# Kernel tuning notes

Hardware: AMD Instinct MI355X
Metric: run time of the kernel (lower is better)

## Reference

```python
import jax, jax.numpy as jnp
import numpy as np
import math

D_MODEL = 1024
NUM_HEADS = 16
HEAD_DIM = D_MODEL // NUM_HEADS  # 64
THETA = 10000.0
BATCH = 2
SEQ = 2048


def setup_inputs() -> dict:
    key = jax.random.key(0)
    ks = jax.random.split(key, 5)
    scale = 0.02
    return {
        "in_features": jax.random.normal(ks[0], (BATCH, SEQ, D_MODEL), jnp.float32),
        "q_proj": jax.random.normal(ks[1], (D_MODEL, D_MODEL), jnp.float32) * scale,
        "k_proj": jax.random.normal(ks[2], (D_MODEL, D_MODEL), jnp.float32) * scale,
        "v_proj": jax.random.normal(ks[3], (D_MODEL, D_MODEL), jnp.float32) * scale,
        "o_proj": jax.random.normal(ks[4], (D_MODEL, D_MODEL), jnp.float32) * scale,
        "token_positions": jnp.arange(SEQ, dtype=jnp.int32),
    }


def _rope(x, token_positions):
    # x: [b, h, s, head_dim]; interleaved even/odd rotation
    half = HEAD_DIM // 2
    inv_freq = 1.0 / (THETA ** (2.0 * jnp.arange(half, dtype=x.dtype) / HEAD_DIM))
    angle = token_positions.astype(x.dtype)[:, None] * inv_freq[None, :]  # [s, half]
    cos, sin = jnp.cos(angle), jnp.sin(angle)
    x_e, x_o = x[..., ::2], x[..., 1::2]
    r_e = x_e * cos - x_o * sin
    r_o = x_e * sin + x_o * cos
    # interleave back: [..., s, half, 2] -> [..., s, head_dim]
    return jnp.stack([r_e, r_o], axis=-1).reshape(x.shape)


def reference(in_features, q_proj, k_proj, v_proj, o_proj, token_positions):
    b, s, _ = in_features.shape
    # projections: weight layout is [d_out, d_in]
    Q = jnp.einsum('bsd,kd->bsk', in_features, q_proj)
    K = jnp.einsum('bsd,kd->bsk', in_features, k_proj)
    V = jnp.einsum('bsd,kd->bsk', in_features, v_proj)
    # split heads: [b, h, s, head_dim]
    Q = Q.reshape(b, s, NUM_HEADS, HEAD_DIM).transpose(0, 2, 1, 3)
    K = K.reshape(b, s, NUM_HEADS, HEAD_DIM).transpose(0, 2, 1, 3)
    V = V.reshape(b, s, NUM_HEADS, HEAD_DIM).transpose(0, 2, 1, 3)
    Q = _rope(Q, token_positions)
    K = _rope(K, token_positions)
    scores = jnp.einsum('bhnd,bhmd->bhnm', Q, K) / math.sqrt(HEAD_DIM)
    causal = jnp.tril(jnp.ones((s, s), dtype=bool))  # [s, s]
    scores = jnp.where(causal[None, None], scores, -jnp.inf)
    attn = jax.nn.softmax(scores, axis=-1)
    out = jnp.einsum('bhnm,bhmd->bhnd', attn, V)
    out = out.transpose(0, 2, 1, 3).reshape(b, s, D_MODEL)
    return jnp.einsum('bsv,dv->bsd', out, o_proj)
```

## Files before the change

### kernel.cpp

```cpp
#include <hip/hip_runtime.h>
#include <hip/hip_bf16.h>

#define D_MODEL 1024
#define NHEAD   16
#define HDIM    64
#define SEQQ    2048
#define NBATCH  2
#define MROWS   (NBATCH * SEQQ)

typedef unsigned short u16;
typedef __attribute__((ext_vector_type(8))) short short8;
typedef __attribute__((ext_vector_type(4))) short bf16x4;
typedef __attribute__((ext_vector_type(4))) float floatx4;

__device__ __forceinline__ u16 f2b(float f) {
    union { __hip_bfloat16 h; u16 u; } cv;
    cv.h = __float2bfloat16(f);
    return cv.u;
}
__device__ __forceinline__ float b2f(u16 u) {
    return __uint_as_float(((unsigned int)u) << 16);
}
__device__ __forceinline__ short8 load8(const u16* p) {
    return *reinterpret_cast<const short8*>(p);
}
__device__ __forceinline__ bf16x4 load4v(const u16* p) {
    return *reinterpret_cast<const bf16x4*>(p);
}
__device__ __forceinline__ unsigned pack2(float lo, float hi) {
    return ((unsigned)f2b(hi) << 16) | (unsigned)f2b(lo);
}
__device__ __forceinline__ void async_cp16(const void* g, void* l) {
    __builtin_amdgcn_global_load_lds(
        (const __attribute__((address_space(1))) void*)g,
        (__attribute__((address_space(3))) void*)l, 16, 0, 0);
}

__global__ void cvt_all(const float* __restrict__ X,
                        const float* __restrict__ w0, const float* __restrict__ w1,
                        const float* __restrict__ w2, const float* __restrict__ w3,
                        u16* __restrict__ xo,
                        u16* __restrict__ o0, u16* __restrict__ o1,
                        u16* __restrict__ o2, u16* __restrict__ o3) {
    const int z = blockIdx.y;
    const int n4 = (D_MODEL * D_MODEL) / 4;
    const float* in;
    u16* out;
    if (z < 4) { in = X + (size_t)z * n4 * 4;  out = xo + (size_t)z * n4 * 4; }
    else {
        in  = (z == 4) ? w0 : (z == 5) ? w1 : (z == 6) ? w2 : w3;
        out = (z == 4) ? o0 : (z == 5) ? o1 : (z == 6) ? o2 : o3;
    }
    const int i = blockIdx.x * 256 + threadIdx.x;
    float4 v = reinterpret_cast<const float4*>(in)[i];
    ushort4 o;
    o.x = f2b(v.x); o.y = f2b(v.y); o.z = f2b(v.z); o.w = f2b(v.w);
    reinterpret_cast<ushort4*>(out)[i] = o;
}

__global__ __launch_bounds__(256) void gemm_qkv(
    const u16* __restrict__ A,
    const u16* __restrict__ B0, const u16* __restrict__ B1, const u16* __restrict__ B2,
    u16* __restrict__ C0, u16* __restrict__ C1, u16* __restrict__ C2)
{
    const int K = D_MODEL, N = D_MODEL;
    const u16* Bt = (blockIdx.z == 0) ? B0 : (blockIdx.z == 1 ? B1 : B2);
    u16*       Cp = (blockIdx.z == 0) ? C0 : (blockIdx.z == 1 ? C1 : C2);

    __shared__ __attribute__((aligned(16))) u16 As[128 * 32];
    __shared__ __attribute__((aligned(16))) u16 Bs[128 * 32];

    const int tid  = threadIdx.x;
    const int w    = tid >> 6;
    const int lane = tid & 63;
    const int l15  = lane & 15;
    const int quad = lane >> 4;
    const int wm   = w >> 1, wn = w & 1;
    const int tm   = blockIdx.x * 128, tn = blockIdx.y * 128;

    floatx4 acc[4][4];
#pragma unroll
    for (int i = 0; i < 4; i++)
#pragma unroll
        for (int j = 0; j < 4; j++) {
            floatx4 z = {0.f, 0.f, 0.f, 0.f};
            acc[i][j] = z;
        }

    const int srow = lane >> 2;
    const int scol = (lane & 3) * 8;

    for (int k0 = 0; k0 < K; k0 += 32) {
#pragma unroll
        for (int ch = w; ch < 8; ch += 4) {
            async_cp16(A  + (size_t)(tm + ch * 16 + srow) * K + k0 + scol, &As[ch * 512]);
            async_cp16(Bt + (size_t)(tn + ch * 16 + srow) * K + k0 + scol, &Bs[ch * 512]);
        }
        __syncthreads();

        short8 af[4], bfr[4];
#pragma unroll
        for (int mi = 0; mi < 4; mi++)
            af[mi] = load8(&As[(wm * 64 + mi * 16 + l15) * 32 + quad * 8]);
#pragma unroll
        for (int ni = 0; ni < 4; ni++)
            bfr[ni] = load8(&Bs[(wn * 64 + ni * 16 + l15) * 32 + quad * 8]);
#pragma unroll
        for (int mi = 0; mi < 4; mi++)
#pragma unroll
            for (int ni = 0; ni < 4; ni++)
                acc[mi][ni] = __builtin_amdgcn_mfma_f32_16x16x32_bf16(af[mi], bfr[ni], acc[mi][ni], 0, 0, 0);
        __syncthreads();
    }

#pragma unroll
    for (int mi = 0; mi < 4; mi++)
#pragma unroll
        for (int ni = 0; ni < 4; ni++)
#pragma unroll
            for (int rg = 0; rg < 4; rg++) {
                int row = tm + wm * 64 + mi * 16 + quad * 4 + rg;
                int col = tn + wn * 64 + ni * 16 + l15;
                Cp[(size_t)row * N + col] = f2b(acc[mi][ni][rg]);
            }
}

__global__ void rope_qk(const u16* __restrict__ Qraw, const u16* __restrict__ Kraw,
                        const int* __restrict__ pos, u16* __restrict__ Qt, u16* __restrict__ Kt)
{
    const int gid = blockIdx.x * 256 + threadIdx.x;
    const int j = gid & 31;
    const int s = (gid >> 5) & (SEQQ - 1);
    const int h = (gid >> 16) & (NHEAD - 1);
    const int b = gid >> 20;

    const float p   = (float)pos[s];
    const float inv = expf(-(float)j * (9.210340371976184f / 32.0f));
    float sn, cs;
    sincosf(p * inv, &sn, &cs);

    const size_t ioff = ((size_t)(b * SEQQ + s)) * D_MODEL + h * HDIM + 2 * j;
    const ushort2 qp = *reinterpret_cast<const ushort2*>(&Qraw[ioff]);
    const ushort2 kp = *reinterpret_cast<const ushort2*>(&Kraw[ioff]);
    const float qe = b2f(qp.x), qo = b2f(qp.y);
    const float ke = b2f(kp.x), ko = b2f(kp.y);

    const size_t ooff = (((size_t)(b * NHEAD + h)) * SEQQ + s) * HDIM + 2 * j;
    const float qs = 0.18033688011112042f;
    ushort2 qr;
    qr.x = f2b((qe * cs - qo * sn) * qs);
    qr.y = f2b((qe * sn + qo * cs) * qs);
    ushort2 kr;
    kr.x = f2b(ke * cs - ko * sn);
    kr.y = f2b(ke * sn + ko * cs);
    *reinterpret_cast<ushort2*>(&Qt[ooff]) = qr;
    *reinterpret_cast<ushort2*>(&Kt[ooff]) = kr;
}

__global__ __launch_bounds__(256) void vtrans(const u16* __restrict__ Vraw, u16* __restrict__ Vt)
{
    __shared__ u16 tile[64][65];
    const int s0 = blockIdx.x * 64, h = blockIdx.y, b = blockIdx.z;
    const int t = threadIdx.x;
#pragma unroll
    for (int i = 0; i < 16; i++) {
        int idx = t + i * 256;
        int sl = idx >> 6, dl = idx & 63;
        tile[sl][dl] = Vraw[((size_t)(b * SEQQ + s0 + sl)) * D_MODEL + h * HDIM + dl];
    }
    __syncthreads();
#pragma unroll
    for (int i = 0; i < 16; i++) {
        int idx = t + i * 256;
        int dl = idx >> 6, sl = idx & 63;
        Vt[(((size_t)(b * NHEAD + h)) * HDIM + dl) * SEQQ + s0 + sl] = tile[sl][dl];
    }
}

__global__ __launch_bounds__(256, 4) void attn_kernel(
    const u16* __restrict__ Qt, const u16* __restrict__ Kt, const u16* __restrict__ Vt,
    u16* __restrict__ Out)
{
    const int bid = blockIdx.x;
    const int xcd = bid & 7;
    const int u   = bid >> 3;
    const int col = xcd * 4 + (u & 3);
    const int m   = u >> 2;
    int qsub;
    if      (m < 8)  qsub = 31 - m;
    else if (m < 16) qsub = m - 8;
    else if (m < 24) qsub = 39 - m;
    else             qsub = m - 16;
    const int h = col & (NHEAD - 1), b = col >> 4;

    const int tid = threadIdx.x, w = tid >> 6, lane = tid & 63;
    const int l15 = lane & 15, quad = lane >> 4;
    const size_t bh = (size_t)(b * NHEAD + h);
    const u16* Qh = Qt + bh * SEQQ * HDIM;
    const u16* Kh = Kt + bh * SEQQ * HDIM;
    const u16* Vh = Vt + bh * HDIM * SEQQ;

    __shared__ __attribute__((aligned(16))) u16 Ks[2][64 * 64];
    __shared__ __attribute__((aligned(16))) u16 Vs[2][64 * 64];

    short8 ones;
#pragma unroll
    for (int i = 0; i < 8; i++) ones[i] = (short)0x3F80;

    const int rr  = lane >> 3;
    const int swz = ((lane & 7) ^ rr) * 8;
    auto stage = [&](int buf, int tt) {
        const int k0s = tt * 64;
        async_cp16(Kh + (size_t)(k0s + w * 8 + rr) * HDIM + swz,       &Ks[buf][w * 512]);
        async_cp16(Kh + (size_t)(k0s + (w + 4) * 8 + rr) * HDIM + swz, &Ks[buf][(w + 4) * 512]);
        async_cp16(Vh + (size_t)(w * 8 + rr) * SEQQ + k0s + swz,       &Vs[buf][w * 512]);
        async_cp16(Vh + (size_t)((w + 4) * 8 + rr) * SEQQ + k0s + swz, &Vs[buf][(w + 4) * 512]);
    };

    const int s7  = l15 & 7;
    const int sw1 = ((quad)     ^ s7) * 8;
    const int sw2 = ((quad + 4) ^ s7) * 8;
    const int vo0 = (((quad >> 1)    ) ^ s7) * 8 + (quad & 1) * 4;
    const int vo1 = (((quad >> 1) + 2) ^ s7) * 8 + (quad & 1) * 4;
    const int vo2 = (((quad >> 1) + 4) ^ s7) * 8 + (quad & 1) * 4;
    const int vo3 = (((quad >> 1) + 6) ^ s7) * 8 + (quad & 1) * 4;

    const int q0w   = qsub * 64 + w * 16;
    const int tmaxp = qsub;

    short8 qf[2];
#pragma unroll
    for (int kk = 0; kk < 2; kk++)
        qf[kk] = load8(&Qh[(size_t)(q0w + l15) * HDIM + kk * 32 + quad * 8]);

    floatx4 O[4];
    floatx4 l_acc = {0.f, 0.f, 0.f, 0.f};
#pragma unroll
    for (int c = 0; c < 4; c++) { floatx4 z = {0.f, 0.f, 0.f, 0.f}; O[c] = z; }

    stage(0, 0);

    for (int t = 0; t <= tmaxp; ++t) {
        asm volatile("s_waitcnt vmcnt(0)" ::: "memory");
        __builtin_amdgcn_s_barrier();
        if (t < tmaxp) stage((t + 1) & 1, t + 1);

        const u16* KsB = &Ks[t & 1][0];
        const u16* VsB = &Vs[t & 1][0];
        const int k0 = t * 64;

        floatx4 S[4];
#pragma unroll
        for (int c = 0; c < 4; c++) {
            const int rowb = (c * 16 + l15) * 64;
            floatx4 z = {0.f, 0.f, 0.f, 0.f};
            S[c] = __builtin_amdgcn_mfma_f32_16x16x32_bf16(load8(&KsB[rowb + sw1]), qf[0], z,    0, 0, 0);
            S[c] = __builtin_amdgcn_mfma_f32_16x16x32_bf16(load8(&KsB[rowb + sw2]), qf[1], S[c], 0, 0, 0);
        }

        if (t == tmaxp) {
            const int q = q0w + l15;
#pragma unroll
            for (int c = 0; c < 4; c++)
#pragma unroll
                for (int r = 0; r < 4; r++)
                    if (k0 + c * 16 + quad * 4 + r > q) S[c][r] = -1e30f;
        }

#pragma unroll
        for (int c = 0; c < 4; c++)
#pragma unroll
            for (int r = 0; r < 4; r++)
                S[c][r] = __builtin_amdgcn_exp2f(S[c][r]);

        union { short8 v; unsigned u[4]; } pf0, pf1;
        pf0.u[0] = pack2(S[0][0], S[0][1]);
        pf0.u[1] = pack2(S[0][2], S[0][3]);
        pf0.u[2] = pack2(S[1][0], S[1][1]);
        pf0.u[3] = pack2(S[1][2], S[1][3]);
        pf1.u[0] = pack2(S[2][0], S[2][1]);
        pf1.u[1] = pack2(S[2][2], S[2][3]);
        pf1.u[2] = pack2(S[3][0], S[3][1]);
        pf1.u[3] = pack2(S[3][2], S[3][3]);

        l_acc = __builtin_amdgcn_mfma_f32_16x16x32_bf16(pf0.v, ones, l_acc, 0, 0, 0);
        l_acc = __builtin_amdgcn_mfma_f32_16x16x32_bf16(pf1.v, ones, l_acc, 0, 0, 0);

#pragma unroll
        for (int c2 = 0; c2 < 4; c2++) {
            const int rowb = (c2 * 16 + l15) * 64;
            bf16x4 a0 = load4v(&VsB[rowb + vo0]);
            bf16x4 a1 = load4v(&VsB[rowb + vo1]);
            bf16x4 a2 = load4v(&VsB[rowb + vo2]);
            bf16x4 a3 = load4v(&VsB[rowb + vo3]);
            short8 v0 = __builtin_shufflevector(a0, a1, 0, 1, 2, 3, 4, 5, 6, 7);
            short8 v1 = __builtin_shufflevector(a2, a3, 0, 1, 2, 3, 4, 5, 6, 7);
            O[c2] = __builtin_amdgcn_mfma_f32_16x16x32_bf16(pf0.v, v0, O[c2], 0, 0, 0);
            O[c2] = __builtin_amdgcn_mfma_f32_16x16x32_bf16(pf1.v, v1, O[c2], 0, 0, 0);
        }
    }

    float inv_l[4];
#pragma unroll
    for (int r = 0; r < 4; r++) inv_l[r] = 1.0f / l_acc[r];

#pragma unroll
    for (int c2 = 0; c2 < 4; c2++)
#pragma unroll
        for (int r = 0; r < 4; r++) {
            const int q    = q0w + quad * 4 + r;
            const int colo = h * HDIM + c2 * 16 + l15;
            Out[(size_t)(b * SEQQ + q) * D_MODEL + colo] = f2b(O[c2][r] * inv_l[r]);
        }
}

__global__ __launch_bounds__(256) void gemm_o(
    const u16* __restrict__ A, const u16* __restrict__ Bt, float* __restrict__ C)
{
    const int K = D_MODEL, N = D_MODEL;
    __shared__ __attribute__((aligned(16))) u16 As[64 * 32];
    __shared__ __attribute__((aligned(16))) u16 Bs[128 * 32];

    const int tid  = threadIdx.x;
    const int w    = tid >> 6;
    const int lane = tid & 63;
    const int l15  = lane & 15;
    const int quad = lane >> 4;
    const int wm   = w >> 1, wn = w & 1;
    const int tm   = blockIdx.x * 64, tn = blockIdx.y * 128;

    floatx4 acc[2][4];
#pragma unroll
    for (int i = 0; i < 2; i++)
#pragma unroll
        for (int j = 0; j < 4; j++) {
            floatx4 z = {0.f, 0.f, 0.f, 0.f};
            acc[i][j] = z;
        }

    const int srow = lane >> 2;
    const int scol = (lane & 3) * 8;

    for (int k0 = 0; k0 < K; k0 += 32) {
#pragma unroll
        for (int ch = w; ch < 12; ch += 4) {
            if (ch < 4) async_cp16(A  + (size_t)(tm + ch * 16 + srow) * K + k0 + scol, &As[ch * 512]);
            else        async_cp16(Bt + (size_t)(tn + (ch - 4) * 16 + srow) * K + k0 + scol, &Bs[(ch - 4) * 512]);
        }
        __syncthreads();

        short8 af[2], bfr[4];
#pragma unroll
        for (int mi = 0; mi < 2; mi++)
            af[mi] = load8(&As[(wm * 32 + mi * 16 + l15) * 32 + quad * 8]);
#pragma unroll
        for (int ni = 0; ni < 4; ni++)
            bfr[ni] = load8(&Bs[(wn * 64 + ni * 16 + l15) * 32 + quad * 8]);
#pragma unroll
        for (int mi = 0; mi < 2; mi++)
#pragma unroll
            for (int ni = 0; ni < 4; ni++)
                acc[mi][ni] = __builtin_amdgcn_mfma_f32_16x16x32_bf16(af[mi], bfr[ni], acc[mi][ni], 0, 0, 0);
        __syncthreads();
    }

#pragma unroll
    for (int mi = 0; mi < 2; mi++)
#pragma unroll
        for (int ni = 0; ni < 4; ni++)
#pragma unroll
            for (int rg = 0; rg < 4; rg++) {
                int row = tm + wm * 32 + mi * 16 + quad * 4 + rg;
                int col = tn + wn * 64 + ni * 16 + l15;
                C[(size_t)row * N + col] = acc[mi][ni][rg];
            }
}

extern "C" void kernel_launch(void* const* d_in, const int* in_sizes, int n_in,
                              void* d_out, int out_size, void* d_ws, size_t ws_size,
                              hipStream_t stream)
{
    const float* X  = (const float*)d_in[0];
    const float* Wq = (const float*)d_in[1];
    const float* Wk = (const float*)d_in[2];
    const float* Wv = (const float*)d_in[3];
    const float* Wo = (const float*)d_in[4];
    const int* tpos = (const int*)d_in[5];
    float* out = (float*)d_out;
    char* ws = (char*)d_ws;

    const size_t MB = (size_t)1 << 20;
    u16* Xb   = (u16*)(ws + 0);
    u16* WqB  = (u16*)(ws + 8 * MB);
    u16* WkB  = (u16*)(ws + 10 * MB);
    u16* WvB  = (u16*)(ws + 12 * MB);
    u16* WoB  = (u16*)(ws + 14 * MB);
    u16* Qraw = (u16*)(ws + 16 * MB);
    u16* Kraw = (u16*)(ws + 24 * MB);
    u16* Vraw = (u16*)(ws + 32 * MB);
    u16* Qt   = (u16*)(ws + 40 * MB);
    u16* Kt   = (u16*)(ws + 48 * MB);
    u16* Vt   = Xb;
    u16* AOut = Qraw;

    cvt_all<<<dim3(1024, 8), 256, 0, stream>>>(X, Wq, Wk, Wv, Wo,
                                               Xb, WqB, WkB, WvB, WoB);

    gemm_qkv<<<dim3(32, 8, 3), 256, 0, stream>>>(Xb, WqB, WkB, WvB,
                                                 Qraw, Kraw, Vraw);
    rope_qk<<<8192, 256, 0, stream>>>(Qraw, Kraw, tpos, Qt, Kt);
    vtrans<<<dim3(32, 16, 2), 256, 0, stream>>>(Vraw, Vt);
    attn_kernel<<<dim3(1024, 1, 1), 256, 0, stream>>>(Qt, Kt, Vt, AOut);
    gemm_o<<<dim3(64, 8), 256, 0, stream>>>(AOut, WoB, out);
}
```

Measured before the change: 185.2 us.

## Fuse RoPE and V transpose into QKV GEMM epilogue with precomputed sin/cos table

```diff
diff --git a/kernel.cpp b/kernel.cpp
--- a/kernel.cpp
+++ b/kernel.cpp
@@ -39,10 +39,24 @@
 __global__ void cvt_all(const float* __restrict__ X,
                         const float* __restrict__ w0, const float* __restrict__ w1,
                         const float* __restrict__ w2, const float* __restrict__ w3,
+                        const int* __restrict__ pos,
                         u16* __restrict__ xo,
                         u16* __restrict__ o0, u16* __restrict__ o1,
-                        u16* __restrict__ o2, u16* __restrict__ o3) {
+                        u16* __restrict__ o2, u16* __restrict__ o3,
+                        float2* __restrict__ tab) {
     const int z = blockIdx.y;
+    if (z == 8) {
+        const int i = blockIdx.x * 256 + threadIdx.x;
+        if (i < SEQQ * 32) {
+            const int s = i >> 5, j = i & 31;
+            const float p = (float)pos[s];
+            const float inv = expf(-(float)j * (9.210340371976184f / 32.0f));
+            float sn, cs;
+            sincosf(p * inv, &sn, &cs);
+            tab[i] = make_float2(cs, sn);
+        }
+        return;
+    }
     const int n4 = (D_MODEL * D_MODEL) / 4;
     const float* in;
     u16* out;
@@ -61,11 +75,12 @@
 __global__ __launch_bounds__(256) void gemm_qkv(
     const u16* __restrict__ A,
     const u16* __restrict__ B0, const u16* __restrict__ B1, const u16* __restrict__ B2,
-    u16* __restrict__ C0, u16* __restrict__ C1, u16* __restrict__ C2)
+    u16* __restrict__ Qt, u16* __restrict__ Kt, u16* __restrict__ Vt,
+    const float2* __restrict__ tab)
 {
-    const int K = D_MODEL, N = D_MODEL;
-    const u16* Bt = (blockIdx.z == 0) ? B0 : (blockIdx.z == 1 ? B1 : B2);
-    u16*       Cp = (blockIdx.z == 0) ? C0 : (blockIdx.z == 1 ? C1 : C2);
+    const int K = D_MODEL;
+    const int z = blockIdx.z;
+    const u16* Bt = (z == 0) ? B0 : (z == 1 ? B1 : B2);
 
     __shared__ __attribute__((aligned(16))) u16 As[128 * 32];
     __shared__ __attribute__((aligned(16))) u16 Bs[128 * 32];
@@ -83,8 +98,8 @@
     for (int i = 0; i < 4; i++)
 #pragma unroll
         for (int j = 0; j < 4; j++) {
-            floatx4 z = {0.f, 0.f, 0.f, 0.f};
-            acc[i][j] = z;
+            floatx4 zz = {0.f, 0.f, 0.f, 0.f};
+            acc[i][j] = zz;
         }
 
     const int srow = lane >> 2;
@@ -113,67 +128,52 @@
         __syncthreads();
     }
 
-#pragma unroll
-    for (int mi = 0; mi < 4; mi++)
-#pragma unroll
-        for (int ni = 0; ni < 4; ni++)
-#pragma unroll
-            for (int rg = 0; rg < 4; rg++) {
-                int row = tm + wm * 64 + mi * 16 + quad * 4 + rg;
-                int col = tn + wn * 64 + ni * 16 + l15;
-                Cp[(size_t)row * N + col] = f2b(acc[mi][ni][rg]);
+    if (z == 2) {
+#pragma unroll
+        for (int mi = 0; mi < 4; mi++) {
+            const int r0 = tm + wm * 64 + mi * 16 + quad * 4;
+            const int bb = r0 >> 11, s0 = r0 & (SEQQ - 1);
+#pragma unroll
+            for (int ni = 0; ni < 4; ni++) {
+                const int colb = tn + wn * 64 + ni * 16 + l15;
+                const int d = colb & 63, hh = colb >> 6;
+                ushort4 pk;
+                pk.x = f2b(acc[mi][ni][0]);
+                pk.y = f2b(acc[mi][ni][1]);
+                pk.z = f2b(acc[mi][ni][2]);
+                pk.w = f2b(acc[mi][ni][3]);
+                *reinterpret_cast<ushort4*>(
+                    &Vt[(((size_t)(bb * NHEAD + hh)) * HDIM + d) * SEQQ + s0]) = pk;
             }
-}
-
-__global__ void rope_qk(const u16* __restrict__ Qraw, const u16* __restrict__ Kraw,
-                        const int* __restrict__ pos, u16* __restrict__ Qt, u16* __restrict__ Kt)
-{
-    const int gid = blockIdx.x * 256 + threadIdx.x;
-    const int j = gid & 31;
-    const int s = (gid >> 5) & (SEQQ - 1);
-    const int h = (gid >> 16) & (NHEAD - 1);
-    const int b = gid >> 20;
-
-    const float p   = (float)pos[s];
-    const float inv = expf(-(float)j * (9.210340371976184f / 32.0f));
-    float sn, cs;
-    sincosf(p * inv, &sn, &cs);
-
-    const size_t ioff = ((size_t)(b * SEQQ + s)) * D_MODEL + h * HDIM + 2 * j;
-    const ushort2 qp = *reinterpret_cast<const ushort2*>(&Qraw[ioff]);
-    const ushort2 kp = *reinterpret_cast<const ushort2*>(&Kraw[ioff]);
-    const float qe = b2f(qp.x), qo = b2f(qp.y);
-    const float ke = b2f(kp.x), ko = b2f(kp.y);
-
-    const size_t ooff = (((size_t)(b * NHEAD + h)) * SEQQ + s) * HDIM + 2 * j;
-    const float qs = 0.18033688011112042f;
-    ushort2 qr;
-    qr.x = f2b((qe * cs - qo * sn) * qs);
-    qr.y = f2b((qe * sn + qo * cs) * qs);
-    ushort2 kr;
-    kr.x = f2b(ke * cs - ko * sn);
-    kr.y = f2b(ke * sn + ko * cs);
-    *reinterpret_cast<ushort2*>(&Qt[ooff]) = qr;
-    *reinterpret_cast<ushort2*>(&Kt[ooff]) = kr;
-}
-
-__global__ __launch_bounds__(256) void vtrans(const u16* __restrict__ Vraw, u16* __restrict__ Vt)
-{
-    __shared__ u16 tile[64][65];
-    const int s0 = blockIdx.x * 64, h = blockIdx.y, b = blockIdx.z;
-    const int t = threadIdx.x;
-#pragma unroll
-    for (int i = 0; i < 16; i++) {
-        int idx = t + i * 256;
-        int sl = idx >> 6, dl = idx & 63;
-        tile[sl][dl] = Vraw[((size_t)(b * SEQQ + s0 + sl)) * D_MODEL + h * HDIM + dl];
-    }
-    __syncthreads();
-#pragma unroll
-    for (int i = 0; i < 16; i++) {
-        int idx = t + i * 256;
-        int dl = idx >> 6, sl = idx & 63;
-        Vt[(((size_t)(b * NHEAD + h)) * HDIM + dl) * SEQQ + s0 + sl] = tile[sl][dl];
+        }
+    } else {
+        const float qsc = (z == 0) ? 0.18033688011112042f : 1.0f;
+        u16* Outp = (z == 0) ? Qt : Kt;
+#pragma unroll
+        for (int mi = 0; mi < 4; mi++) {
+            const int r0 = tm + wm * 64 + mi * 16 + quad * 4;
+#pragma unroll
+            for (int ni = 0; ni < 4; ni++) {
+                const int colb = tn + wn * 64 + ni * 16 + l15;
+                const int d = colb & 63, hh = colb >> 6;
+                const int j = d >> 1;
+                const bool odd = (d & 1) != 0;
+#pragma unroll
+                for (int rg = 0; rg < 4; rg++) {
+                    const int r = r0 + rg;
+                    const int bb = r >> 11, s = r & (SEQQ - 1);
+                    const float own = acc[mi][ni][rg];
+                    const float oth = __shfl_xor(own, 1);
+                    const float2 cs = tab[s * 32 + j];
+                    const float xe = odd ? oth : own;
+                    const float xo = odd ? own : oth;
+                    const float res = odd ? (xe * cs.y + xo * cs.x)
+                                          : (xe * cs.x - xo * cs.y);
+                    Outp[(((size_t)(bb * NHEAD + hh)) * SEQQ + s) * HDIM + d] =
+                        f2b(res * qsc);
+                }
+            }
+        }
     }
 }
 
@@ -236,7 +236,7 @@
     floatx4 O[4];
     floatx4 l_acc = {0.f, 0.f, 0.f, 0.f};
 #pragma unroll
-    for (int c = 0; c < 4; c++) { floatx4 z = {0.f, 0.f, 0.f, 0.f}; O[c] = z; }
+    for (int c = 0; c < 4; c++) { floatx4 zz = {0.f, 0.f, 0.f, 0.f}; O[c] = zz; }
 
     stage(0, 0);
 
@@ -253,8 +253,8 @@
 #pragma unroll
         for (int c = 0; c < 4; c++) {
             const int rowb = (c * 16 + l15) * 64;
-            floatx4 z = {0.f, 0.f, 0.f, 0.f};
-            S[c] = __builtin_amdgcn_mfma_f32_16x16x32_bf16(load8(&KsB[rowb + sw1]), qf[0], z,    0, 0, 0);
+            floatx4 zz = {0.f, 0.f, 0.f, 0.f};
+            S[c] = __builtin_amdgcn_mfma_f32_16x16x32_bf16(load8(&KsB[rowb + sw1]), qf[0], zz,   0, 0, 0);
             S[c] = __builtin_amdgcn_mfma_f32_16x16x32_bf16(load8(&KsB[rowb + sw2]), qf[1], S[c], 0, 0, 0);
         }
 
@@ -390,26 +390,22 @@
     char* ws = (char*)d_ws;
 
     const size_t MB = (size_t)1 << 20;
-    u16* Xb   = (u16*)(ws + 0);
-    u16* WqB  = (u16*)(ws + 8 * MB);
-    u16* WkB  = (u16*)(ws + 10 * MB);
-    u16* WvB  = (u16*)(ws + 12 * MB);
-    u16* WoB  = (u16*)(ws + 14 * MB);
-    u16* Qraw = (u16*)(ws + 16 * MB);
-    u16* Kraw = (u16*)(ws + 24 * MB);
-    u16* Vraw = (u16*)(ws + 32 * MB);
-    u16* Qt   = (u16*)(ws + 40 * MB);
-    u16* Kt   = (u16*)(ws + 48 * MB);
-    u16* Vt   = Xb;
-    u16* AOut = Qraw;
-
-    cvt_all<<<dim3(1024, 8), 256, 0, stream>>>(X, Wq, Wk, Wv, Wo,
-                                               Xb, WqB, WkB, WvB, WoB);
+    u16*    Xb  = (u16*)(ws + 0);
+    u16*    WqB = (u16*)(ws + 8 * MB);
+    u16*    WkB = (u16*)(ws + 10 * MB);
+    u16*    WvB = (u16*)(ws + 12 * MB);
+    u16*    WoB = (u16*)(ws + 14 * MB);
+    float2* tab = (float2*)(ws + 16 * MB);
+    u16*    Qt  = (u16*)(ws + 24 * MB);
+    u16*    Kt  = (u16*)(ws + 32 * MB);
+    u16*    Vt  = (u16*)(ws + 40 * MB);
+    u16*   AOut = (u16*)(ws + 48 * MB);
+
+    cvt_all<<<dim3(1024, 9), 256, 0, stream>>>(X, Wq, Wk, Wv, Wo, tpos,
+                                               Xb, WqB, WkB, WvB, WoB, tab);
 
     gemm_qkv<<<dim3(32, 8, 3), 256, 0, stream>>>(Xb, WqB, WkB, WvB,
-                                                 Qraw, Kraw, Vraw);
-    rope_qk<<<8192, 256, 0, stream>>>(Qraw, Kraw, tpos, Qt, Kt);
-    vtrans<<<dim3(32, 16, 2), 256, 0, stream>>>(Vraw, Vt);
+                                                 Qt, Kt, Vt, tab);
     attn_kernel<<<dim3(1024, 1, 1), 256, 0, stream>>>(Qt, Kt, Vt, AOut);
     gemm_o<<<dim3(64, 8), 256, 0, stream>>>(AOut, WoB, out);
 }
```

New measurement: 190.0 us. 2.6% more time.
